# Kernel tuning notes

Hardware: AMD Instinct MI355X
Metric: run time of the kernel (lower is better)

## Reference

```python
import jax, jax.numpy as jnp
import numpy as np

K = 16
ITERS = 5
DIST_CHUNK = 8  # feature-chunk size to avoid materializing [B,F,S,S]


def pairwise_l1(x):
    """x: [B, F, S] -> d: [B, S, S], d[b,i,j] = ||x[b,:,i]-x[b,:,j]||_1.
    Computed in feature chunks via scan so peak intermediate is [B,CH,S,S]."""
    B, F, S = x.shape
    xc = x.reshape(B, F // DIST_CHUNK, DIST_CHUNK, S).transpose(1, 0, 2, 3)  # [F/CH,B,CH,S]

    def step(acc, blk):  # blk: [B, CH, S]
        return acc + jnp.abs(blk[:, :, :, None] - blk[:, :, None, :]).sum(axis=1), None

    d, _ = jax.lax.scan(step, jnp.zeros((B, S, S), x.dtype), xc)
    return d


def kmedoids_pool(x, w):
    B, F, S = x.shape
    wm = jnp.mean(w, axis=1)                       # [B,S] per-token attention weight
    d = pairwise_l1(x)                             # [B,S,S]
    _, ctr = jax.lax.top_k(wm, K)                  # [B,K] initial medoids
    dw = d * wm[:, None, :]                        # d[b,i,j]*w[b,j]
    for _ in range(ITERS):
        # distance from every token to each current medoid: [B,S,K]
        i2c = jnp.take_along_axis(d, jnp.broadcast_to(ctr[:, None, :], (B, S, K)), axis=2)
        assign = jnp.argmin(i2c, axis=2)           # [B,S] cluster assignment
        member = jax.nn.one_hot(assign, K, dtype=x.dtype)  # [B,S,K]
        # weighted within-cluster cost for candidate i in cluster k:
        # cost[b,i,k] = sum_j d[b,i,j]*w[b,j]*member[b,j,k]
        cost = jnp.einsum('bij,bjk->bik', dw, member)
        cost = jnp.where(member > 0, cost, jnp.inf)  # medoid must be a member
        ctr = jnp.argmin(cost, axis=1)             # [B,K] new medoids
    idx = jnp.broadcast_to(ctr[:, None, :], (B, F, K))
    return jnp.take_along_axis(x, idx, axis=2)     # [B,F,K]


def setup_inputs() -> dict:
    key = jax.random.key(0)
    kx, kw = jax.random.split(key)
    B, F, S = 8, 256, 1024
    x = jax.random.normal(kx, (B, F, S), dtype=jnp.float32)
    w = jax.random.uniform(kw, (B, S, S), dtype=jnp.float32)
    return {"x": x, "w": w}


def reference(x, w):
    return kmedoids_pool(x, w)
```

## Files before the change

### kernel.cpp

```cpp
#include <hip/hip_runtime.h>
#include <math.h>

#define BB 8
#define FF 256
#define SS 1024
#define KK 16
#define ITERS 5

typedef unsigned long long ull;

#define ICH 8
__global__ void wm_part_kernel(const float* __restrict__ w, float* __restrict__ part) {
    int j = blockIdx.x * 256 + threadIdx.x;
    int ic = blockIdx.y, b = blockIdx.z;
    const float* wp = w + (size_t)b * SS * SS + (size_t)ic * (SS / ICH) * SS + j;
    float s = 0.f;
#pragma unroll 8
    for (int i = 0; i < SS / ICH; ++i) s += wp[(size_t)i * SS];
    part[((size_t)ic * BB + b) * SS + j] = s;
}

__global__ void wm_final_kernel(const float* __restrict__ part, float* __restrict__ wm) {
    int t = blockIdx.x * blockDim.x + threadIdx.x;
    if (t >= BB * SS) return;
    int b = t / SS, j = t % SS;
    float s = 0.f;
#pragma unroll
    for (int ic = 0; ic < ICH; ++ic) s += part[((size_t)ic * BB + b) * SS + j];
    wm[t] = s * (1.0f / SS);
}

#define FCD 16
__device__ __forceinline__ void async_copy16(const float* g, const float* s) {
    __builtin_amdgcn_global_load_lds((const __attribute__((address_space(1))) void*)g,
                                     (__attribute__((address_space(3))) void*)s, 16, 0, 0);
}

__global__ __launch_bounds__(64, 4) void dist_kernel(const float* __restrict__ x,
                                                     float* __restrict__ d) {
    __shared__ float smem[2048];
    int lane = threadIdx.x;
    int b = blockIdx.y;
    int w = blockIdx.x;
    int it = 0, rem = w;
    while (rem >= 32 - it) { rem -= 32 - it; ++it; }
    int jt = it + rem;
    int i0 = it * 32, j0 = jt * 32;
    const float* xb = x + (size_t)b * FF * SS;
    float* db = d + (size_t)b * SS * SS;
    int ly = lane >> 3, lx = lane & 7;
    int sFl = lane >> 3, sTk = (lane & 7) * 4;

    float acc[4][4] = {};

    auto stage = [&](int c, int h) {
        float* A = smem + h * 1024;
        float* B = A + 512;
        const float* base = xb + (size_t)c * FCD * SS;
#pragma unroll
        for (int ci = 0; ci < 2; ++ci) {
            async_copy16(base + (size_t)(ci * 8 + sFl) * SS + i0 + sTk, A + ci * 256);
            async_copy16(base + (size_t)(ci * 8 + sFl) * SS + j0 + sTk, B + ci * 256);
        }
    };
    auto compute = [&](int h) {
        const float* A = smem + h * 1024;
        const float* B = A + 512;
#pragma unroll 4
        for (int f = 0; f < FCD; ++f) {
            float4 a = *(const float4*)(A + f * 32 + ly * 4);
            float4 bb = *(const float4*)(B + f * 32 + lx * 4);
            float av[4] = {a.x, a.y, a.z, a.w};
            float bv[4] = {bb.x, bb.y, bb.z, bb.w};
#pragma unroll
            for (int r = 0; r < 4; ++r)
#pragma unroll
                for (int c = 0; c < 4; ++c)
                    acc[r][c] += fabsf(av[r] - bv[c]);
        }
    };

    stage(0, 0);
#pragma unroll 1
    for (int k = 0; k < FF / FCD - 1; ++k) {
        asm volatile("s_waitcnt lgkmcnt(0)" ::: "memory");
        stage(k + 1, (k + 1) & 1);
        asm volatile("s_waitcnt vmcnt(4)" ::: "memory");
        compute(k & 1);
    }
    asm volatile("s_waitcnt vmcnt(0)" ::: "memory");
    compute(1);

#pragma unroll
    for (int r = 0; r < 4; ++r) {
        float4 v = make_float4(acc[r][0], acc[r][1], acc[r][2], acc[r][3]);
        *(float4*)&db[(size_t)(i0 + ly * 4 + r) * SS + j0 + lx * 4] = v;
    }
    if (it != jt) {
#pragma unroll
        for (int c = 0; c < 4; ++c) {
            float4 v = make_float4(acc[0][c], acc[1][c], acc[2][c], acc[3][c]);
            *(float4*)&db[(size_t)(j0 + lx * 4 + c) * SS + i0 + ly * 4] = v;
        }
    }
}

__global__ __launch_bounds__(1024) void topk_assign_kernel(const float* __restrict__ wm,
                                                           const float* __restrict__ d,
                                                           int* __restrict__ assign) {
    int b = blockIdx.x;
    int tid = threadIdx.x;
    int lane = tid & 63, wv = tid >> 6;
    __shared__ ull red[16];
    __shared__ int ctr_s[KK];
    float v = wm[b * SS + tid];
    ull key = (((ull)__float_as_uint(v)) << 32) | (ull)(0xFFFFFFFFu - (unsigned)tid);
    for (int k = 0; k < KK; ++k) {
        ull kk = key;
#pragma unroll
        for (int off = 32; off; off >>= 1) {
            ull o = __shfl_down(kk, off, 64);
            if (o > kk) kk = o;
        }
        if (lane == 0) red[wv] = kk;
        __syncthreads();
        if (wv == 0) {
            ull k2 = (lane < 16) ? red[lane] : 0ull;
#pragma unroll
            for (int off = 8; off; off >>= 1) {
                ull o = __shfl_down(k2, off, 64);
                if (o > k2) k2 = o;
            }
            if (lane == 0) red[0] = k2;
        }
        __syncthreads();
        ull W = red[0];
        int widx = (int)(0xFFFFFFFFu - (unsigned)(W & 0xFFFFFFFFu));
        if (tid == widx) key = 0;
        if (tid == 0) ctr_s[k] = widx;
        __syncthreads();
    }
    const float* db = d + (size_t)b * SS * SS;
    float bv = INFINITY;
    int bk = 0;
#pragma unroll
    for (int k = 0; k < KK; ++k) {
        float vv = db[(size_t)ctr_s[k] * SS + tid];
        if (vv < bv) { bv = vv; bk = k; }
    }
    assign[b * SS + tid] = bk;
}

__global__ __launch_bounds__(256) void cost_kernel(const float* __restrict__ d,
                                                   const float* __restrict__ wm,
                                                   const int* __restrict__ assign,
                                                   float* __restrict__ cost) {
    int b = blockIdx.y;
    int i = blockIdx.x;
    int tid = threadIdx.x;
    int my = assign[b * SS + i];
    const float* drow = d + (size_t)b * SS * SS + (size_t)i * SS;
    const float* wb = wm + b * SS;
    const int* ab = assign + b * SS;
    float4 dv = *(const float4*)&drow[tid * 4];
    float4 wv = *(const float4*)&wb[tid * 4];
    int4 av = *(const int4*)&ab[tid * 4];
    float s = 0.f;
    s += (av.x == my) ? dv.x * wv.x : 0.f;
    s += (av.y == my) ? dv.y * wv.y : 0.f;
    s += (av.z == my) ? dv.z * wv.z : 0.f;
    s += (av.w == my) ? dv.w * wv.w : 0.f;
#pragma unroll
    for (int off = 32; off > 0; off >>= 1) s += __shfl_down(s, off, 64);
    __shared__ float ws_s[4];
    if ((tid & 63) == 0) ws_s[tid >> 6] = s;
    __syncthreads();
    if (tid == 0) cost[b * SS + i] = (ws_s[0] + ws_s[1]) + (ws_s[2] + ws_s[3]);
}

__global__ __launch_bounds__(1024) void update_assign_kernel(
        const float* __restrict__ d, const float* __restrict__ cost,
        int* __restrict__ assign, const float* __restrict__ x,
        float* __restrict__ out, int last) {
    int b = blockIdx.x;
    int tid = threadIdx.x;
    int lane = tid & 63, wv = tid >> 6;
    __shared__ float cost_s[SS];
    __shared__ int assign_s[SS];
    __shared__ int ctr_s[KK];
    cost_s[tid] = cost[b * SS + tid];
    assign_s[tid] = assign[b * SS + tid];
    __syncthreads();
    ull best = ~0ull;
    int k = wv;
    for (int c = 0; c < SS / 64; ++c) {
        int i = c * 64 + lane;
        if (assign_s[i] == k) {
            ull key = (((ull)__float_as_uint(cost_s[i])) << 32) | (unsigned)i;
            if (key < best) best = key;
        }
    }
#pragma unroll
    for (int off = 32; off; off >>= 1) {
        ull o = __shfl_down(best, off, 64);
        if (o < best) best = o;
    }
    if (lane == 0) ctr_s[k] = (best == ~0ull) ? 0 : (int)(best & 0xFFFFFFFFu);
    __syncthreads();
    if (!last) {
        const float* db = d + (size_t)b * SS * SS;
        float bv = INFINITY;
        int bk = 0;
#pragma unroll
        for (int k2 = 0; k2 < KK; ++k2) {
            float vv = db[(size_t)ctr_s[k2] * SS + tid];
            if (vv < bv) { bv = vv; bk = k2; }
        }
        assign[b * SS + tid] = bk;
    } else {
        for (int e = tid; e < FF * KK; e += 1024) {
            int f = e / KK, k2 = e % KK;
            out[((size_t)b * FF + f) * KK + k2] = x[((size_t)b * FF + f) * SS + ctr_s[k2]];
        }
    }
}

extern "C" void kernel_launch(void* const* d_in, const int* in_sizes, int n_in,
                              void* d_out, int out_size, void* d_ws, size_t ws_size,
                              hipStream_t stream) {
    const float* x = (const float*)d_in[0];
    const float* w = (const float*)d_in[1];
    float* out = (float*)d_out;

    char* ws = (char*)d_ws;
    float* d = (float*)ws;
    size_t off = (size_t)BB * SS * SS * sizeof(float);
    float* wm = (float*)(ws + off);  off += (size_t)BB * SS * sizeof(float);
    int* assign = (int*)(ws + off);  off += (size_t)BB * SS * sizeof(int);
    float* cost = (float*)(ws + off);
    float* part = (float*)ws;

    wm_part_kernel<<<dim3(SS / 256, ICH, BB), 256, 0, stream>>>(w, part);
    wm_final_kernel<<<(BB * SS + 255) / 256, 256, 0, stream>>>(part, wm);
    dist_kernel<<<dim3(528, BB), 64, 0, stream>>>(x, d);
    topk_assign_kernel<<<BB, 1024, 0, stream>>>(wm, d, assign);
    for (int itr = 0; itr < ITERS; ++itr) {
        cost_kernel<<<dim3(SS, BB), 256, 0, stream>>>(d, wm, assign, cost);
        update_assign_kernel<<<BB, 1024, 0, stream>>>(d, cost, assign, x, out,
                                                      itr == ITERS - 1 ? 1 : 0);
    }
}
```

Baseline: 240.3 us.

## Fuse wm finalize into top-k, pack two waves per dist block, split update across blocks

Removes the wm_final kernel by folding the partial-sum reduction into topk_assign. dist_kernel now packs two 64-lane tiles per 128-thread block, and each wave stages only 8 features per buffer with its own half of shared memory. update_assign now runs on 4 blocks per batch, and each block recomputes the medoids redundantly before splitting the assignment (k-groups reduced through shared memory) or the output gather. It also gives part its own workspace slot so it no longer aliases d. The aim is fewer launches and more parallelism in the small serial kernels, at the cost of redundant medoid work and shorter pipeline stages in dist.

```diff
diff --git a/kernel.cpp b/kernel.cpp
--- a/kernel.cpp
+++ b/kernel.cpp
@@ -20,53 +20,41 @@
     part[((size_t)ic * BB + b) * SS + j] = s;
 }
 
-__global__ void wm_final_kernel(const float* __restrict__ part, float* __restrict__ wm) {
-    int t = blockIdx.x * blockDim.x + threadIdx.x;
-    if (t >= BB * SS) return;
-    int b = t / SS, j = t % SS;
-    float s = 0.f;
-#pragma unroll
-    for (int ic = 0; ic < ICH; ++ic) s += part[((size_t)ic * BB + b) * SS + j];
-    wm[t] = s * (1.0f / SS);
-}
-
-#define FCD 16
+#define FCD 8
 __device__ __forceinline__ void async_copy16(const float* g, const float* s) {
     __builtin_amdgcn_global_load_lds((const __attribute__((address_space(1))) void*)g,
                                      (__attribute__((address_space(3))) void*)s, 16, 0, 0);
 }
 
-__global__ __launch_bounds__(64, 4) void dist_kernel(const float* __restrict__ x,
-                                                     float* __restrict__ d) {
+__global__ __launch_bounds__(128, 8) void dist_kernel(const float* __restrict__ x,
+                                                      float* __restrict__ d) {
     __shared__ float smem[2048];
-    int lane = threadIdx.x;
+    int tid = threadIdx.x;
+    int wave = tid >> 6, lane = tid & 63;
     int b = blockIdx.y;
-    int w = blockIdx.x;
+    int w = blockIdx.x * 2 + wave;
     int it = 0, rem = w;
     while (rem >= 32 - it) { rem -= 32 - it; ++it; }
     int jt = it + rem;
     int i0 = it * 32, j0 = jt * 32;
     const float* xb = x + (size_t)b * FF * SS;
     float* db = d + (size_t)b * SS * SS;
+    float* wbase = smem + wave * 1024;
     int ly = lane >> 3, lx = lane & 7;
     int sFl = lane >> 3, sTk = (lane & 7) * 4;
 
     float acc[4][4] = {};
 
     auto stage = [&](int c, int h) {
-        float* A = smem + h * 1024;
-        float* B = A + 512;
-        const float* base = xb + (size_t)c * FCD * SS;
-#pragma unroll
-        for (int ci = 0; ci < 2; ++ci) {
-            async_copy16(base + (size_t)(ci * 8 + sFl) * SS + i0 + sTk, A + ci * 256);
-            async_copy16(base + (size_t)(ci * 8 + sFl) * SS + j0 + sTk, B + ci * 256);
-        }
+        float* A = wbase + h * 512;
+        const float* base = xb + (size_t)c * FCD * SS + (size_t)sFl * SS;
+        async_copy16(base + i0 + sTk, A);
+        async_copy16(base + j0 + sTk, A + 256);
     };
     auto compute = [&](int h) {
-        const float* A = smem + h * 1024;
-        const float* B = A + 512;
-#pragma unroll 4
+        const float* A = wbase + h * 512;
+        const float* B = A + 256;
+#pragma unroll
         for (int f = 0; f < FCD; ++f) {
             float4 a = *(const float4*)(A + f * 32 + ly * 4);
             float4 bb = *(const float4*)(B + f * 32 + lx * 4);
@@ -85,7 +73,7 @@
     for (int k = 0; k < FF / FCD - 1; ++k) {
         asm volatile("s_waitcnt lgkmcnt(0)" ::: "memory");
         stage(k + 1, (k + 1) & 1);
-        asm volatile("s_waitcnt vmcnt(4)" ::: "memory");
+        asm volatile("s_waitcnt vmcnt(2)" ::: "memory");
         compute(k & 1);
     }
     asm volatile("s_waitcnt vmcnt(0)" ::: "memory");
@@ -105,7 +93,8 @@
     }
 }
 
-__global__ __launch_bounds__(1024) void topk_assign_kernel(const float* __restrict__ wm,
+__global__ __launch_bounds__(1024) void topk_assign_kernel(const float* __restrict__ part,
+                                                           float* __restrict__ wm,
                                                            const float* __restrict__ d,
                                                            int* __restrict__ assign) {
     int b = blockIdx.x;
@@ -113,7 +102,11 @@
     int lane = tid & 63, wv = tid >> 6;
     __shared__ ull red[16];
     __shared__ int ctr_s[KK];
-    float v = wm[b * SS + tid];
+    float v = 0.f;
+#pragma unroll
+    for (int ic = 0; ic < ICH; ++ic) v += part[((size_t)ic * BB + b) * SS + tid];
+    v *= (1.0f / SS);
+    wm[b * SS + tid] = v;
     ull key = (((ull)__float_as_uint(v)) << 32) | (ull)(0xFFFFFFFFu - (unsigned)tid);
     for (int k = 0; k < KK; ++k) {
         ull kk = key;
@@ -182,12 +175,14 @@
         const float* __restrict__ d, const float* __restrict__ cost,
         int* __restrict__ assign, const float* __restrict__ x,
         float* __restrict__ out, int last) {
-    int b = blockIdx.x;
+    int b = blockIdx.y;
+    int q = blockIdx.x;
     int tid = threadIdx.x;
     int lane = tid & 63, wv = tid >> 6;
     __shared__ float cost_s[SS];
     __shared__ int assign_s[SS];
     __shared__ int ctr_s[KK];
+    __shared__ ull pk[4][256];
     cost_s[tid] = cost[b * SS + tid];
     assign_s[tid] = assign[b * SS + tid];
     __syncthreads();
@@ -207,21 +202,31 @@
     }
     if (lane == 0) ctr_s[k] = (best == ~0ull) ? 0 : (int)(best & 0xFFFFFFFFu);
     __syncthreads();
+    const float* db = d + (size_t)b * SS * SS;
     if (!last) {
-        const float* db = d + (size_t)b * SS * SS;
-        float bv = INFINITY;
-        int bk = 0;
-#pragma unroll
-        for (int k2 = 0; k2 < KK; ++k2) {
-            float vv = db[(size_t)ctr_s[k2] * SS + tid];
-            if (vv < bv) { bv = vv; bk = k2; }
-        }
-        assign[b * SS + tid] = bk;
+        int tok = q * 256 + (tid & 255);
+        int g = tid >> 8;
+        ull bk = ~0ull;
+#pragma unroll
+        for (int kk = 0; kk < 4; ++kk) {
+            int k2 = g * 4 + kk;
+            float vv = db[(size_t)ctr_s[k2] * SS + tok];
+            ull key = (((ull)__float_as_uint(vv)) << 32) | (unsigned)k2;
+            if (key < bk) bk = key;
+        }
+        pk[g][tid & 255] = bk;
+        __syncthreads();
+        if (tid < 256) {
+            ull m = pk[0][tid];
+            if (pk[1][tid] < m) m = pk[1][tid];
+            if (pk[2][tid] < m) m = pk[2][tid];
+            if (pk[3][tid] < m) m = pk[3][tid];
+            assign[b * SS + q * 256 + tid] = (int)(m & 0xFFFFFFFFu);
+        }
     } else {
-        for (int e = tid; e < FF * KK; e += 1024) {
-            int f = e / KK, k2 = e % KK;
-            out[((size_t)b * FF + f) * KK + k2] = x[((size_t)b * FF + f) * SS + ctr_s[k2]];
-        }
+        int e = q * 1024 + tid;
+        int f = e / KK, k2 = e % KK;
+        out[((size_t)b * FF + f) * KK + k2] = x[((size_t)b * FF + f) * SS + ctr_s[k2]];
     }
 }
 
@@ -235,18 +240,17 @@
     char* ws = (char*)d_ws;
     float* d = (float*)ws;
     size_t off = (size_t)BB * SS * SS * sizeof(float);
-    float* wm = (float*)(ws + off);  off += (size_t)BB * SS * sizeof(float);
-    int* assign = (int*)(ws + off);  off += (size_t)BB * SS * sizeof(int);
-    float* cost = (float*)(ws + off);
-    float* part = (float*)ws;
+    float* wm = (float*)(ws + off);   off += (size_t)BB * SS * sizeof(float);
+    int* assign = (int*)(ws + off);   off += (size_t)BB * SS * sizeof(int);
+    float* cost = (float*)(ws + off); off += (size_t)BB * SS * sizeof(float);
+    float* part = (float*)(ws + off);
 
     wm_part_kernel<<<dim3(SS / 256, ICH, BB), 256, 0, stream>>>(w, part);
-    wm_final_kernel<<<(BB * SS + 255) / 256, 256, 0, stream>>>(part, wm);
-    dist_kernel<<<dim3(528, BB), 64, 0, stream>>>(x, d);
-    topk_assign_kernel<<<BB, 1024, 0, stream>>>(wm, d, assign);
+    dist_kernel<<<dim3(264, BB), 128, 0, stream>>>(x, d);
+    topk_assign_kernel<<<BB, 1024, 0, stream>>>(part, wm, d, assign);
     for (int itr = 0; itr < ITERS; ++itr) {
         cost_kernel<<<dim3(SS, BB), 256, 0, stream>>>(d, wm, assign, cost);
-        update_assign_kernel<<<BB, 1024, 0, stream>>>(d, cost, assign, x, out,
-                                                      itr == ITERS - 1 ? 1 : 0);
-    }
-}
+        update_assign_kernel<<<dim3(4, BB), 1024, 0, stream>>>(d, cost, assign, x, out,
+                                                               itr == ITERS - 1 ? 1 : 0);
+    }
+}
```

After: 329.8 us. 1.37x slower.
